# Performance work log

Hardware: AMD Instinct MI355X
Metric: run time of the kernel (lower is better)

Reference implementation:

```python
import jax, jax.numpy as jnp
import numpy as np

N = 10000      # nodes
E = 160000     # edges (before self loops)
G = 16         # graphs in batch
H = 4          # attention heads
F = 128        # hidden_dim (per-head out channels)
DIN = 64       # input_dim
NEG_SLOPE = 0.2


def setup_inputs() -> dict:
    key = jax.random.key(0)
    ks = jax.random.split(key, 20)
    x = jax.random.normal(ks[0], (N, DIN), jnp.float32)
    edge_index = jax.random.randint(ks[1], (2, E), 0, N, jnp.int32)
    batch = jnp.sort(jax.random.randint(ks[2], (N,), 0, G, jnp.int32))

    def p(k, shape, scale):
        return (jax.random.normal(k, shape, jnp.float32) * scale).astype(jnp.float32)

    ins = [DIN, H * F, H * F]
    params = {}
    for i in range(3):
        d = ins[i]
        params[f"W{i}"] = p(ks[3 + 4 * i], (d, H * F), (2.0 / (d + F)) ** 0.5)
        params[f"as{i}"] = p(ks[4 + 4 * i], (H, F), 0.1)
        params[f"ad{i}"] = p(ks[5 + 4 * i], (H, F), 0.1)
        bdim = H * F if i < 2 else F
        params[f"b{i}"] = jnp.zeros((bdim,), jnp.float32)
    params["Wr1"] = p(ks[15], (F, F), (2.0 / (2 * F)) ** 0.5)
    params["br1"] = jnp.zeros((F,), jnp.float32)
    params["Wr2"] = p(ks[16], (F, 2 * F), (2.0 / (3 * F)) ** 0.5)
    params["br2"] = jnp.zeros((2 * F,), jnp.float32)
    return {"x": x, "edge_index": edge_index, "batch": batch, **params}


def gat_layer(x, src, dst, W, a_s, a_d, b, concat):
    """PyG-style GATConv (eval mode, self loops already in src/dst)."""
    n = x.shape[0]
    h = (x @ W).reshape(n, H, F)                      # [N,H,F]
    e = jax.nn.leaky_relu(((h * a_s).sum(-1))[src] + ((h * a_d).sum(-1))[dst], NEG_SLOPE)  # [E,H]
    m = jax.ops.segment_max(e, dst, num_segments=n)   # segment softmax over dst
    w = jnp.exp(e - m[dst])
    denom = jax.ops.segment_sum(w, dst, num_segments=n)
    alpha = w / denom[dst]                            # [E,H]
    out = jax.ops.segment_sum(alpha[:, :, None] * h[src], dst, num_segments=n)  # [N,H,F]
    out = out.reshape(n, H * F) if concat else out.mean(axis=1)
    return out + b


def reference(x, edge_index, batch, W0, as0, ad0, b0, W1, as1, ad1, b1,
              W2, as2, ad2, b2, Wr1, br1, Wr2, br2):
    n = x.shape[0]
    loops = jnp.arange(n, dtype=edge_index.dtype)     # add_self_loops (PyG default)
    src = jnp.concatenate([edge_index[0], loops])
    dst = jnp.concatenate([edge_index[1], loops])
    h = jax.nn.relu(gat_layer(x, src, dst, W0, as0, ad0, b0, True))
    h = jax.nn.relu(gat_layer(h, src, dst, W1, as1, ad1, b1, True))
    h = gat_layer(h, src, dst, W2, as2, ad2, b2, False)   # [N,F]
    # global mean pool over graphs
    sums = jax.ops.segment_sum(h, batch, num_segments=G)
    cnt = jax.ops.segment_sum(jnp.ones((n, 1), h.dtype), batch, num_segments=G)
    g = sums / jnp.maximum(cnt, 1.0)                   # [G,F]
    z = jax.nn.relu(g @ Wr1 + br1)
    return z @ Wr2 + br2                               # [G,256]
```

## Files before the change

### kernel.cpp

```cpp
#include <hip/hip_runtime.h>
#include <hip/hip_bf16.h>
#include <math.h>

constexpr int NN  = 10000;
constexpr int NE  = 160000;
constexpr int GG  = 16;
constexpr int HH  = 4;
constexpr int FF  = 128;
constexpr int HF  = 512;

typedef __attribute__((ext_vector_type(8))) short bf16x8;
typedef __attribute__((ext_vector_type(4))) float f32x4;

__device__ inline short f2bf(float v) {
    __hip_bfloat16 h = __float2bfloat16(v);
    return *reinterpret_cast<short*>(&h);
}
__device__ inline float bf2f(short s) {
    __hip_bfloat16 h = *reinterpret_cast<__hip_bfloat16*>(&s);
    return __bfloat162float(h);
}

__global__ __launch_bounds__(1024) void histo_scan(const int* __restrict__ ei,
                                                   int* __restrict__ offsets,
                                                   int* __restrict__ cursor,
                                                   float* __restrict__ sums) {
    __shared__ int hist[NN];
    __shared__ int wsum[16];
    __shared__ int carry;
    int tid = threadIdx.x, lane = tid & 63, wv = tid >> 6;
    for (int i = tid; i < NN; i += 1024) hist[i] = 0;
    for (int i = tid; i < GG * FF; i += 1024) sums[i] = 0.f;
    if (tid == 0) carry = 0;
    __syncthreads();
    for (int e = tid; e < NE; e += 1024) atomicAdd(&hist[ei[NE + e]], 1);
    __syncthreads();
    for (int base = 0; base < NN; base += 1024) {
        int i = base + tid;
        int v = (i < NN) ? hist[i] : 0;
        int x = v;
#pragma unroll
        for (int st = 1; st < 64; st <<= 1) {
            int t = __shfl_up(x, st);
            if (lane >= st) x += t;
        }
        if (lane == 63) wsum[wv] = x;
        __syncthreads();
        if (tid == 0) {
            int s = carry;
            for (int k2 = 0; k2 < 16; k2++) { int t = wsum[k2]; wsum[k2] = s; s += t; }
            carry = s;
        }
        __syncthreads();
        int excl = wsum[wv] + x - v;
        if (i < NN) { offsets[i] = excl; cursor[i] = excl; }
        __syncthreads();
    }
    if (tid == 0) offsets[NN] = carry;
}

__global__ __launch_bounds__(256) void prep_scatter(const float* __restrict__ x,
                                                    short* __restrict__ xb,
                                                    const float* __restrict__ W0,
                                                    const float* __restrict__ W1,
                                                    const float* __restrict__ W2,
                                                    short* __restrict__ T0,
                                                    short* __restrict__ T1,
                                                    short* __restrict__ T2,
                                                    const int* __restrict__ ei,
                                                    int* __restrict__ cursor,
                                                    int* __restrict__ adj) {
    int z = blockIdx.z;
    int tid = threadIdx.x;
    int bid = blockIdx.y * 16 + blockIdx.x;
    if (z == 3) {
        const float4* x4 = (const float4*)x;
        for (int i = bid * 256 + tid; i < NN * 16; i += 256 * 256) {
            float4 v = x4[i];
            short4 o;
            o.x = f2bf(v.x); o.y = f2bf(v.y); o.z = f2bf(v.z); o.w = f2bf(v.w);
            *(short4*)&xb[i * 4] = o;
        }
        return;
    }
    if (z == 4) {
        for (int e = bid * 256 + tid; e < NE; e += 256 * 256) {
            int dst = ei[NE + e];
            int pos = atomicAdd(&cursor[dst], 1);
            adj[pos] = ei[e];
        }
        return;
    }
    const float* W = (z == 0) ? W0 : (z == 1) ? W1 : W2;
    short* T = (z == 0) ? T0 : (z == 1) ? T1 : T2;
    int K = (z == 0) ? 64 : HF;
    int bn = blockIdx.x * 32, bk = blockIdx.y * 32;
    if (bk >= K) return;
    __shared__ float tile[32][33];
    int tx = tid & 31, ty = tid >> 5;
    for (int r = ty; r < 32; r += 8) {
        int k = bk + r, n = bn + tx;
        tile[r][tx] = W[(size_t)k * HF + n];
    }
    __syncthreads();
    for (int r = ty; r < 32; r += 8) {
        int n = bn + r, k = bk + tx;
        T[(size_t)n * K + k] = f2bf(tile[tx][r]);
    }
}

__global__ __launch_bounds__(256) void gemm_attn(const short* __restrict__ A,
                                                 const short* __restrict__ B,
                                                 short* __restrict__ Cb,
                                                 float* __restrict__ es,
                                                 float* __restrict__ ed,
                                                 const float* __restrict__ a_s,
                                                 const float* __restrict__ a_d,
                                                 int M, int K) {
    constexpr int BM = 64, BK = 32, LDT = BK + 8;
    __shared__ short As[BM][LDT];
    __shared__ short Bh[FF][LDT];
    __shared__ float s_red[4][BM][2];
    int tid = threadIdx.x;
    int wave = tid >> 6, lane = tid & 63;
    int fr = lane & 15, fq = lane >> 4;
    int bm = blockIdx.x * BM;
    int head = blockIdx.y;
    int bn = head * FF;
    int arow = tid >> 2, acol = (tid & 3) * 8;
    int brow = tid >> 1, bcol = (tid & 1) * 16;
    f32x4 acc[4][2] = {};
    for (int k0 = 0; k0 < K; k0 += BK) {
        {
            int row = bm + arow;
            bf16x8 va = {};
            if (row < M) va = *(const bf16x8*)&A[(size_t)row * K + k0 + acol];
            *(bf16x8*)&As[arow][acol] = va;
            const short* bsh = &B[(size_t)(bn + brow) * K + k0 + bcol];
            *(bf16x8*)&Bh[brow][bcol]     = *(const bf16x8*)bsh;
            *(bf16x8*)&Bh[brow][bcol + 8] = *(const bf16x8*)(bsh + 8);
        }
        __syncthreads();
        bf16x8 af[4], bh[2];
#pragma unroll
        for (int m = 0; m < 4; m++)
            af[m] = *(const bf16x8*)&As[m * 16 + fr][fq * 8];
#pragma unroll
        for (int n = 0; n < 2; n++)
            bh[n] = *(const bf16x8*)&Bh[wave * 32 + n * 16 + fr][fq * 8];
#pragma unroll
        for (int m = 0; m < 4; m++)
#pragma unroll
            for (int n = 0; n < 2; n++)
                acc[m][n] = __builtin_amdgcn_mfma_f32_16x16x32_bf16(af[m], bh[n], acc[m][n], 0, 0, 0);
        __syncthreads();
    }
    float asv[2], adv[2];
#pragma unroll
    for (int n = 0; n < 2; n++) {
        int c = wave * 32 + n * 16 + fr;
        asv[n] = a_s[head * FF + c];
        adv[n] = a_d[head * FF + c];
    }
#pragma unroll
    for (int m = 0; m < 4; m++) {
#pragma unroll
        for (int j = 0; j < 4; j++) {
            float ps = 0.f, pd = 0.f;
#pragma unroll
            for (int n = 0; n < 2; n++) {
                float v = acc[m][n][j];
                ps += v * asv[n];
                pd += v * adv[n];
            }
#pragma unroll
            for (int o = 1; o < 16; o <<= 1) {
                ps += __shfl_xor(ps, o);
                pd += __shfl_xor(pd, o);
            }
            int rloc = m * 16 + fq * 4 + j;
            if (fr == 0) { s_red[wave][rloc][0] = ps; s_red[wave][rloc][1] = pd; }
            int row = bm + rloc;
            if (row < M) {
#pragma unroll
                for (int n = 0; n < 2; n++)
                    Cb[(size_t)row * HF + bn + wave * 32 + n * 16 + fr] = f2bf(acc[m][n][j]);
            }
        }
    }
    __syncthreads();
    if (tid < BM) {
        int row = bm + tid;
        if (row < M) {
            es[row * 4 + head] = s_red[0][tid][0] + s_red[1][tid][0] +
                                 s_red[2][tid][0] + s_red[3][tid][0];
            ed[row * 4 + head] = s_red[0][tid][1] + s_red[1][tid][1] +
                                 s_red[2][tid][1] + s_red[3][tid][1];
        }
    }
}

template <int MODE>
__global__ __launch_bounds__(256) void gat_aggregate(const short* __restrict__ h,
                                                     const float* __restrict__ es,
                                                     const float* __restrict__ ed,
                                                     const int* __restrict__ offsets,
                                                     const int* __restrict__ adj,
                                                     const float* __restrict__ bias,
                                                     float* __restrict__ outf,
                                                     short* __restrict__ outb) {
    constexpr int CAP = 64;
    __shared__ int s_src[4][CAP];
    __shared__ float s_wt[4][4][CAP];
    int tid = threadIdx.x, w = tid >> 6, lane = tid & 63;
    int n = blockIdx.x * 4 + w;
    int row0 = offsets[n];
    int deg = offsets[n + 1] - row0;
    int tot = min(deg + 1, CAP);
    if (lane < tot)
        s_src[w][lane] = (lane < deg) ? adj[row0 + lane] : n;
    float4 edv = *(const float4*)&ed[n * 4];
    float mx0 = -1e30f, mx1 = -1e30f, mx2 = -1e30f, mx3 = -1e30f;
    if (lane < tot) {
        int s = s_src[w][lane];
        float4 e4 = *(const float4*)&es[s * 4];
        float e0 = e4.x + edv.x; e0 = (e0 >= 0.f) ? e0 : 0.2f * e0;
        float e1 = e4.y + edv.y; e1 = (e1 >= 0.f) ? e1 : 0.2f * e1;
        float e2 = e4.z + edv.z; e2 = (e2 >= 0.f) ? e2 : 0.2f * e2;
        float e3 = e4.w + edv.w; e3 = (e3 >= 0.f) ? e3 : 0.2f * e3;
        s_wt[w][0][lane] = e0; s_wt[w][1][lane] = e1;
        s_wt[w][2][lane] = e2; s_wt[w][3][lane] = e3;
        mx0 = e0; mx1 = e1; mx2 = e2; mx3 = e3;
    }
#pragma unroll
    for (int o = 1; o < 64; o <<= 1) {
        mx0 = fmaxf(mx0, __shfl_xor(mx0, o));
        mx1 = fmaxf(mx1, __shfl_xor(mx1, o));
        mx2 = fmaxf(mx2, __shfl_xor(mx2, o));
        mx3 = fmaxf(mx3, __shfl_xor(mx3, o));
    }
    float s0 = 0.f, s1 = 0.f, s2 = 0.f, s3 = 0.f;
    if (lane < tot) {
        float v0 = __expf(s_wt[w][0][lane] - mx0); s_wt[w][0][lane] = v0; s0 = v0;
        float v1 = __expf(s_wt[w][1][lane] - mx1); s_wt[w][1][lane] = v1; s1 = v1;
        float v2 = __expf(s_wt[w][2][lane] - mx2); s_wt[w][2][lane] = v2; s2 = v2;
        float v3 = __expf(s_wt[w][3][lane] - mx3); s_wt[w][3][lane] = v3; s3 = v3;
    }
#pragma unroll
    for (int o = 1; o < 64; o <<= 1) {
        s0 += __shfl_xor(s0, o); s1 += __shfl_xor(s1, o);
        s2 += __shfl_xor(s2, o); s3 += __shfl_xor(s3, o);
    }
    __syncthreads();
    int head = lane >> 4;
    float rd = 1.f / ((head == 0) ? s0 : (head == 1) ? s1 : (head == 2) ? s2 : s3);
    float acc[8] = {};
    const short* hbase = h + lane * 8;
    for (int i = 0; i < tot; i++) {
        int s = s_src[w][i];
        float wt = s_wt[w][head][i];
        bf16x8 hv = *(const bf16x8*)&hbase[(size_t)s * HF];
#pragma unroll
        for (int k = 0; k < 8; k++) acc[k] += wt * bf2f(hv[k]);
    }
#pragma unroll
    for (int k = 0; k < 8; k++) acc[k] *= rd;
    if (MODE == 0) {
        int c = lane * 8;
        float4 b0 = *(const float4*)&bias[c];
        float4 b1 = *(const float4*)&bias[c + 4];
        bf16x8 o;
        o[0] = f2bf(fmaxf(acc[0] + b0.x, 0.f));
        o[1] = f2bf(fmaxf(acc[1] + b0.y, 0.f));
        o[2] = f2bf(fmaxf(acc[2] + b0.z, 0.f));
        o[3] = f2bf(fmaxf(acc[3] + b0.w, 0.f));
        o[4] = f2bf(fmaxf(acc[4] + b1.x, 0.f));
        o[5] = f2bf(fmaxf(acc[5] + b1.y, 0.f));
        o[6] = f2bf(fmaxf(acc[6] + b1.z, 0.f));
        o[7] = f2bf(fmaxf(acc[7] + b1.w, 0.f));
        *(bf16x8*)&outb[(size_t)n * HF + c] = o;
    } else {
#pragma unroll
        for (int k = 0; k < 8; k++) {
            acc[k] += __shfl_xor(acc[k], 16);
            acc[k] += __shfl_xor(acc[k], 32);
        }
        if (lane < 16) {
            int c = lane * 8;
#pragma unroll
            for (int k = 0; k < 8; k++)
                outf[(size_t)n * FF + c + k] = 0.25f * acc[k] + bias[c + k];
        }
    }
}

__global__ __launch_bounds__(128) void pool_kernel(const float* __restrict__ h2,
                                                   const int* __restrict__ batch,
                                                   float* __restrict__ sums) {
    int f = threadIdx.x;
    int start = blockIdx.x * 64;
    float acc = 0.f;
    int curg = -1;
    for (int i = 0; i < 64; i++) {
        int node = start + i;
        if (node >= NN) break;
        int g = batch[node];
        if (g != curg) {
            if (curg >= 0) atomicAdd(&sums[curg * FF + f], acc);
            acc = 0.f;
            curg = g;
        }
        acc += h2[(size_t)node * FF + f];
    }
    if (curg >= 0) atomicAdd(&sums[curg * FF + f], acc);
}

__global__ __launch_bounds__(256) void mlp_kernel(const float* __restrict__ sums,
                                                  const int* __restrict__ batch,
                                                  const float* __restrict__ Wr1,
                                                  const float* __restrict__ br1,
                                                  const float* __restrict__ Wr2,
                                                  const float* __restrict__ br2,
                                                  float* __restrict__ out) {
    int g = blockIdx.x, t = threadIdx.x;
    __shared__ float gv[128];
    __shared__ float z[128];
    __shared__ float cinv;
    if (t == 0) {
        auto lb = [&](int key) {
            int lo = 0, hi = NN;
            while (lo < hi) { int mid = (lo + hi) >> 1; if (batch[mid] < key) lo = mid + 1; else hi = mid; }
            return lo;
        };
        int cnt = lb(g + 1) - lb(g);
        cinv = 1.0f / fmaxf((float)cnt, 1.0f);
    }
    __syncthreads();
    if (t < 128) gv[t] = sums[g * FF + t] * cinv;
    __syncthreads();
    if (t < 128) {
        float a = br1[t];
        for (int k = 0; k < 128; k++) a += gv[k] * Wr1[k * 128 + t];
        z[t] = fmaxf(a, 0.f);
    }
    __syncthreads();
    {
        float a = br2[t];
        for (int k = 0; k < 128; k++) a += z[k] * Wr2[k * 256 + t];
        out[g * 256 + t] = a;
    }
}

extern "C" void kernel_launch(void* const* d_in, const int* in_sizes, int n_in,
                              void* d_out, int out_size, void* d_ws, size_t ws_size,
                              hipStream_t stream) {
    const float* x    = (const float*)d_in[0];
    const int*   ei   = (const int*)d_in[1];
    const int*   batch= (const int*)d_in[2];
    const float* W0   = (const float*)d_in[3];
    const float* as0  = (const float*)d_in[4];
    const float* ad0  = (const float*)d_in[5];
    const float* b0   = (const float*)d_in[6];
    const float* W1   = (const float*)d_in[7];
    const float* as1  = (const float*)d_in[8];
    const float* ad1  = (const float*)d_in[9];
    const float* b1   = (const float*)d_in[10];
    const float* W2   = (const float*)d_in[11];
    const float* as2  = (const float*)d_in[12];
    const float* ad2  = (const float*)d_in[13];
    const float* b2   = (const float*)d_in[14];
    const float* Wr1  = (const float*)d_in[15];
    const float* br1  = (const float*)d_in[16];
    const float* Wr2  = (const float*)d_in[17];
    const float* br2  = (const float*)d_in[18];
    float* out = (float*)d_out;

    char* p = (char*)d_ws;
    auto alloc = [&](size_t bytes) {
        char* r = p;
        p += (bytes + 255) / 256 * 256;
        return r;
    };
    short* hA      = (short*)alloc((size_t)NN * HF * 2);
    short* hB      = (short*)alloc((size_t)NN * HF * 2);
    float* h2      = (float*)alloc((size_t)NN * FF * 4);
    short* xb      = (short*)alloc((size_t)NN * 64 * 2);
    short* T0      = (short*)alloc((size_t)HF * 64 * 2);
    short* T1      = (short*)alloc((size_t)HF * HF * 2);
    short* T2      = (short*)alloc((size_t)HF * HF * 2);
    float* es      = (float*)alloc((size_t)NN * HH * 4);
    float* ed      = (float*)alloc((size_t)NN * HH * 4);
    int*   offsets = (int*)alloc((size_t)(NN + 1) * 4);
    int*   cursor  = (int*)alloc((size_t)NN * 4);
    int*   adj     = (int*)alloc((size_t)NE * 4);
    float* sums    = (float*)alloc((size_t)GG * FF * 4);

    histo_scan<<<1, 1024, 0, stream>>>(ei, offsets, cursor, sums);

    prep_scatter<<<dim3(16, 16, 5), 256, 0, stream>>>(x, xb, W0, W1, W2, T0, T1, T2,
                                                      ei, cursor, adj);

    dim3 ggemm((NN + 63) / 64, HH);

    gemm_attn<<<ggemm, 256, 0, stream>>>(xb, T0, hA, es, ed, as0, ad0, NN, 64);
    gat_aggregate<0><<<NN / 4, 256, 0, stream>>>(hA, es, ed, offsets, adj, b0, nullptr, hB);

    gemm_attn<<<ggemm, 256, 0, stream>>>(hB, T1, hA, es, ed, as1, ad1, NN, HF);
    gat_aggregate<0><<<NN / 4, 256, 0, stream>>>(hA, es, ed, offsets, adj, b1, nullptr, hB);

    gemm_attn<<<ggemm, 256, 0, stream>>>(hB, T2, hA, es, ed, as2, ad2, NN, HF);
    gat_aggregate<1><<<NN / 4, 256, 0, stream>>>(hA, es, ed, offsets, adj, b2, h2, nullptr);

    pool_kernel<<<(NN + 63) / 64, 128, 0, stream>>>(h2, batch, sums);
    mlp_kernel<<<GG, 256, 0, stream>>>(sums, batch, Wr1, br1, Wr2, br2, out);
}
```

Baseline: 221.3 us.

## Replace CSR histogram-scan build with fixed-stride padded adjacency lists

The single-block histogram plus prefix-scan kernel that built CSR offsets is dropped. Each node now gets a fixed slot of 64 entries, filled by an atomic degree counter during the scatter, and only a small parallel zeroing kernel runs first. This removes a long serial one-block kernel from the critical path. In exchange, neighbours past 63 are silently dropped and the adjacency buffer grows, though the previous aggregate already capped degree at the same size.

```diff
diff --git a/kernel.cpp b/kernel.cpp
--- a/kernel.cpp
+++ b/kernel.cpp
@@ -8,6 +8,7 @@
 constexpr int HH  = 4;
 constexpr int FF  = 128;
 constexpr int HF  = 512;
+constexpr int DS  = 64;
 
 typedef __attribute__((ext_vector_type(8))) short bf16x8;
 typedef __attribute__((ext_vector_type(4))) float f32x4;
@@ -21,42 +22,11 @@
     return __bfloat162float(h);
 }
 
-__global__ __launch_bounds__(1024) void histo_scan(const int* __restrict__ ei,
-                                                   int* __restrict__ offsets,
-                                                   int* __restrict__ cursor,
+__global__ __launch_bounds__(256) void zero_kernel(int* __restrict__ degs,
                                                    float* __restrict__ sums) {
-    __shared__ int hist[NN];
-    __shared__ int wsum[16];
-    __shared__ int carry;
-    int tid = threadIdx.x, lane = tid & 63, wv = tid >> 6;
-    for (int i = tid; i < NN; i += 1024) hist[i] = 0;
-    for (int i = tid; i < GG * FF; i += 1024) sums[i] = 0.f;
-    if (tid == 0) carry = 0;
-    __syncthreads();
-    for (int e = tid; e < NE; e += 1024) atomicAdd(&hist[ei[NE + e]], 1);
-    __syncthreads();
-    for (int base = 0; base < NN; base += 1024) {
-        int i = base + tid;
-        int v = (i < NN) ? hist[i] : 0;
-        int x = v;
-#pragma unroll
-        for (int st = 1; st < 64; st <<= 1) {
-            int t = __shfl_up(x, st);
-            if (lane >= st) x += t;
-        }
-        if (lane == 63) wsum[wv] = x;
-        __syncthreads();
-        if (tid == 0) {
-            int s = carry;
-            for (int k2 = 0; k2 < 16; k2++) { int t = wsum[k2]; wsum[k2] = s; s += t; }
-            carry = s;
-        }
-        __syncthreads();
-        int excl = wsum[wv] + x - v;
-        if (i < NN) { offsets[i] = excl; cursor[i] = excl; }
-        __syncthreads();
-    }
-    if (tid == 0) offsets[NN] = carry;
+    int i = blockIdx.x * 256 + threadIdx.x;
+    if (i < NN) degs[i] = 0;
+    if (i < GG * FF) sums[i] = 0.f;
 }
 
 __global__ __launch_bounds__(256) void prep_scatter(const float* __restrict__ x,
@@ -68,7 +38,7 @@
                                                     short* __restrict__ T1,
                                                     short* __restrict__ T2,
                                                     const int* __restrict__ ei,
-                                                    int* __restrict__ cursor,
+                                                    int* __restrict__ degs,
                                                     int* __restrict__ adj) {
     int z = blockIdx.z;
     int tid = threadIdx.x;
@@ -86,8 +56,8 @@
     if (z == 4) {
         for (int e = bid * 256 + tid; e < NE; e += 256 * 256) {
             int dst = ei[NE + e];
-            int pos = atomicAdd(&cursor[dst], 1);
-            adj[pos] = ei[e];
+            int pos = atomicAdd(&degs[dst], 1);
+            if (pos < DS) adj[dst * DS + pos] = ei[e];
         }
         return;
     }
@@ -204,21 +174,20 @@
 __global__ __launch_bounds__(256) void gat_aggregate(const short* __restrict__ h,
                                                      const float* __restrict__ es,
                                                      const float* __restrict__ ed,
-                                                     const int* __restrict__ offsets,
+                                                     const int* __restrict__ degs,
                                                      const int* __restrict__ adj,
                                                      const float* __restrict__ bias,
                                                      float* __restrict__ outf,
                                                      short* __restrict__ outb) {
-    constexpr int CAP = 64;
+    constexpr int CAP = DS;
     __shared__ int s_src[4][CAP];
     __shared__ float s_wt[4][4][CAP];
     int tid = threadIdx.x, w = tid >> 6, lane = tid & 63;
     int n = blockIdx.x * 4 + w;
-    int row0 = offsets[n];
-    int deg = offsets[n + 1] - row0;
-    int tot = min(deg + 1, CAP);
+    int deg = min(degs[n], CAP - 1);
+    int tot = deg + 1;
     if (lane < tot)
-        s_src[w][lane] = (lane < deg) ? adj[row0 + lane] : n;
+        s_src[w][lane] = (lane < deg) ? adj[n * DS + lane] : n;
     float4 edv = *(const float4*)&ed[n * 4];
     float mx0 = -1e30f, mx1 = -1e30f, mx2 = -1e30f, mx3 = -1e30f;
     if (lane < tot) {
@@ -390,26 +359,25 @@
     short* T2      = (short*)alloc((size_t)HF * HF * 2);
     float* es      = (float*)alloc((size_t)NN * HH * 4);
     float* ed      = (float*)alloc((size_t)NN * HH * 4);
-    int*   offsets = (int*)alloc((size_t)(NN + 1) * 4);
-    int*   cursor  = (int*)alloc((size_t)NN * 4);
-    int*   adj     = (int*)alloc((size_t)NE * 4);
+    int*   degs    = (int*)alloc((size_t)NN * 4);
+    int*   adj     = (int*)alloc((size_t)NN * DS * 4);
     float* sums    = (float*)alloc((size_t)GG * FF * 4);
 
-    histo_scan<<<1, 1024, 0, stream>>>(ei, offsets, cursor, sums);
+    zero_kernel<<<(NN + 255) / 256, 256, 0, stream>>>(degs, sums);
 
     prep_scatter<<<dim3(16, 16, 5), 256, 0, stream>>>(x, xb, W0, W1, W2, T0, T1, T2,
-                                                      ei, cursor, adj);
+                                                      ei, degs, adj);
 
     dim3 ggemm((NN + 63) / 64, HH);
 
     gemm_attn<<<ggemm, 256, 0, stream>>>(xb, T0, hA, es, ed, as0, ad0, NN, 64);
-    gat_aggregate<0><<<NN / 4, 256, 0, stream>>>(hA, es, ed, offsets, adj, b0, nullptr, hB);
+    gat_aggregate<0><<<NN / 4, 256, 0, stream>>>(hA, es, ed, degs, adj, b0, nullptr, hB);
 
     gemm_attn<<<ggemm, 256, 0, stream>>>(hB, T1, hA, es, ed, as1, ad1, NN, HF);
-    gat_aggregate<0><<<NN / 4, 256, 0, stream>>>(hA, es, ed, offsets, adj, b1, nullptr, hB);
+    gat_aggregate<0><<<NN / 4, 256, 0, stream>>>(hA, es, ed, degs, adj, b1, nullptr, hB);
 
     gemm_attn<<<ggemm, 256, 0, stream>>>(hB, T2, hA, es, ed, as2, ad2, NN, HF);
-    gat_aggregate<1><<<NN / 4, 256, 0, stream>>>(hA, es, ed, offsets, adj, b2, h2, nullptr);
+    gat_aggregate<1><<<NN / 4, 256, 0, stream>>>(hA, es, ed, degs, adj, b2, h2, nullptr);
 
     pool_kernel<<<(NN + 63) / 64, 128, 0, stream>>>(h2, batch, sums);
     mlp_kernel<<<GG, 256, 0, stream>>>(sums, batch, Wr1, br1, Wr2, br2, out);
```

Result: faster. 191.7 us (-13.4%).
